# Kernel tuning notes

Hardware: AMD Instinct MI355X
Metric: run time of the kernel (lower is better)

Reference implementation:

```python
import jax, jax.numpy as jnp
import numpy as np


def setup_inputs() -> dict:
    key = jax.random.key(0)
    kx, ky = jax.random.split(key)
    B, C, T = 4, 2, 32768
    x = jax.random.normal(kx, (B, C, T), dtype=jnp.float32)
    y = jax.random.normal(ky, (B, C, T), dtype=jnp.float32)
    return {"x": x, "y": y, "max_shift": 128}


def reference(x, y, max_shift):
    # x: (B, C, T), y: (B, C, T) (or any suffix shape broadcastable from the right)
    T = x.shape[-1]
    S = 2 * max_shift + 1  # number of shift windows
    # pad last dim by max_shift on each side
    pad_cfg = [(0, 0)] * (x.ndim - 1) + [(max_shift, max_shift)]
    x_pad = jnp.pad(x, pad_cfg)
    # unfold into S overlapping windows of length T, stride 1
    idx = jnp.arange(S)[:, None] + jnp.arange(T)[None, :]  # (S, T)
    xw = x_pad[..., idx]                 # (B, C, S, T)
    xw = jnp.moveaxis(xw, -2, 0)         # (S, B, C, T)
    # center each window and y along time
    xw = xw - xw.mean(-1, keepdims=True)
    yc = y - y.mean(-1, keepdims=True)
    corr = (xw * yc).sum(-1)                               # (S, B, C)
    norm = (xw ** 2).sum(-1) * (yc ** 2).sum(-1)           # (S, B, C)
    return corr / jnp.sqrt(norm)
```

## Files before the change

### kernel.cpp

```cpp
#include <hip/hip_runtime.h>
#include <math.h>

#define MAX_SHIFT 128
#define S_TOTAL   257
#define SGB       9
#define NSB       32
#define BLOCK     1024
#define VY        8
#define NW        (BLOCK / 64)
#define NQ        (SGB + 4)

__global__ __launch_bounds__(BLOCK) void spc_kernel(const float* __restrict__ x,
                                                    const float* __restrict__ y,
                                                    float* __restrict__ out,
                                                    int T, int BC) {
    const int sg  = blockIdx.x;
    const int bc  = blockIdx.y;
    const int s0  = sg * 8;
    const int d0  = s0 - MAX_SHIFT;
    const int tid = threadIdx.x;
    const float* xb = x + (size_t)bc * T;
    const float* yb = y + (size_t)bc * T;

    float acc[SGB];
#pragma unroll
    for (int j = 0; j < SGB; ++j) acc[j] = 0.f;
    float sx = 0.f, sxx = 0.f, sy = 0.f, syy = 0.f;

    for (int t = tid * VY; t < T; t += BLOCK * VY) {
        float yv[VY], xv[VY], xw[16];
        *(float4*)(yv)     = *(const float4*)(yb + t);
        *(float4*)(yv + 4) = *(const float4*)(yb + t + 4);
        *(float4*)(xv)     = *(const float4*)(xb + t);
        *(float4*)(xv + 4) = *(const float4*)(xb + t + 4);

        const int g0 = t + d0;
        if (g0 >= 0 && g0 + 16 <= T) {
#pragma unroll
            for (int i = 0; i < 4; ++i)
                *(float4*)(xw + 4 * i) = *(const float4*)(xb + g0 + 4 * i);
        } else {
#pragma unroll
            for (int i = 0; i < 16; ++i) {
                int g = g0 + i;
                xw[i] = (g >= 0 && g < T) ? xb[g] : 0.f;
            }
        }

#pragma unroll
        for (int e = 0; e < VY; ++e) {
            const float yvv = yv[e];
#pragma unroll
            for (int j = 0; j < SGB; ++j)
                acc[j] = fmaf(xw[e + j], yvv, acc[j]);
            sy += yvv;  syy = fmaf(yvv, yvv, syy);
            sx += xv[e]; sxx = fmaf(xv[e], xv[e], sxx);
        }
    }

    __shared__ float red[NQ][NW];
    __shared__ float tot[NQ];
    __shared__ float edge[SGB][2];
    const int lane = tid & 63, wave = tid >> 6;
#pragma unroll
    for (int j = 0; j < SGB; ++j) {
        float v = acc[j];
        for (int off = 32; off; off >>= 1) v += __shfl_down(v, off, 64);
        if (lane == 0) red[j][wave] = v;
    }
    {
        float v4[4] = {sx, sxx, sy, syy};
#pragma unroll
        for (int q = 0; q < 4; ++q) {
            float v = v4[q];
            for (int off = 32; off; off >>= 1) v += __shfl_down(v, off, 64);
            if (lane == 0) red[SGB + q][wave] = v;
        }
    }

    if (wave < SGB) {
        const int sl = wave;
        int d = d0 + sl;
        float pw = 0.f, pw2 = 0.f;
        if (d > 0) {
            for (int j = lane; j < d; j += 64)  { float v = xb[j];         pw += v; pw2 = fmaf(v, v, pw2); }
        } else if (d < 0) {
            for (int j = lane; j < -d; j += 64) { float v = xb[T + d + j]; pw += v; pw2 = fmaf(v, v, pw2); }
        }
        for (int off = 32; off; off >>= 1) {
            pw  += __shfl_down(pw,  off, 64);
            pw2 += __shfl_down(pw2, off, 64);
        }
        if (lane == 0) { edge[sl][0] = pw; edge[sl][1] = pw2; }
    }
    __syncthreads();

    if (tid < NQ) {
        float v = 0.f;
#pragma unroll
        for (int w = 0; w < NW; ++w) v += red[tid][w];
        tot[tid] = v;
    }
    __syncthreads();

    if (tid < SGB) {
        int s = s0 + tid;
        if (s < S_TOTAL) {
            float cr  = tot[tid];
            float Sx  = tot[SGB + 0];
            float Sxx = tot[SGB + 1];
            float Sy  = tot[SGB + 2];
            float Syy = tot[SGB + 3];
            float Sw  = Sx  - edge[tid][0];
            float Sw2 = Sxx - edge[tid][1];
            float invT  = 1.0f / (float)T;
            float corr  = cr  - Sw * Sy * invT;
            float normx = Sw2 - Sw * Sw * invT;
            float normy = Syy - Sy * Sy * invT;
            out[(size_t)s * BC + bc] = corr / sqrtf(normx * normy);
        }
    }
}

extern "C" void kernel_launch(void* const* d_in, const int* in_sizes, int n_in,
                              void* d_out, int out_size, void* d_ws, size_t ws_size,
                              hipStream_t stream) {
    const float* x = (const float*)d_in[0];
    const float* y = (const float*)d_in[1];
    float* out = (float*)d_out;

    const int BC = out_size / S_TOTAL;
    const int T  = in_sizes[0] / BC;

    dim3 grid(NSB, BC);
    spc_kernel<<<grid, BLOCK, 0, stream>>>(x, y, out, T, BC);
}
```

Baseline: 65.98 us.

## Split time axis across blocks and add a separate reduction kernel

Splits the time dimension into 8 chunks per (shift group, batch-channel) using 256-thread blocks, so the grid grows from 256 large blocks to 2048 smaller ones and fills the GPU better. Per-chunk partial sums go to workspace and a second kernel reduces them and computes the edge corrections per shift. The x/y moments are now computed only by the block with zero shift offset, which removes redundant work in the others. The cost is a second kernel launch plus extra workspace traffic.

```diff
diff --git a/kernel.cpp b/kernel.cpp
--- a/kernel.cpp
+++ b/kernel.cpp
@@ -4,35 +4,37 @@
 #define MAX_SHIFT 128
 #define S_TOTAL   257
 #define SGB       9
-#define NSB       32
-#define BLOCK     1024
+#define NSG       32
 #define VY        8
-#define NW        (BLOCK / 64)
-#define NQ        (SGB + 4)
+#define BLK1      256
+#define NW1       (BLK1/64)
+#define CCH       8
 
-__global__ __launch_bounds__(BLOCK) void spc_kernel(const float* __restrict__ x,
-                                                    const float* __restrict__ y,
-                                                    float* __restrict__ out,
-                                                    int T, int BC) {
+
+__global__ __launch_bounds__(BLK1, 8) void spc_partial(const float* __restrict__ x,
+                                                       const float* __restrict__ y,
+                                                       float* __restrict__ ws,
+                                                       int T, int BC) {
     const int sg  = blockIdx.x;
     const int bc  = blockIdx.y;
-    const int s0  = sg * 8;
-    const int d0  = s0 - MAX_SHIFT;
+    const int ch  = blockIdx.z;
+    const int d0  = sg * 8 - MAX_SHIFT;
     const int tid = threadIdx.x;
     const float* xb = x + (size_t)bc * T;
     const float* yb = y + (size_t)bc * T;
+    const int chunk = T / CCH;
+    const int t0 = ch * chunk;
+    const bool domom = (d0 == 0);
 
     float acc[SGB];
 #pragma unroll
     for (int j = 0; j < SGB; ++j) acc[j] = 0.f;
     float sx = 0.f, sxx = 0.f, sy = 0.f, syy = 0.f;
 
-    for (int t = tid * VY; t < T; t += BLOCK * VY) {
-        float yv[VY], xv[VY], xw[16];
+    for (int t = t0 + tid * VY; t < t0 + chunk; t += BLK1 * VY) {
+        float yv[VY], xw[16];
         *(float4*)(yv)     = *(const float4*)(yb + t);
         *(float4*)(yv + 4) = *(const float4*)(yb + t + 4);
-        *(float4*)(xv)     = *(const float4*)(xb + t);
-        *(float4*)(xv + 4) = *(const float4*)(xb + t + 4);
 
         const int g0 = t + d0;
         if (g0 >= 0 && g0 + 16 <= T) {
@@ -53,14 +55,14 @@
 #pragma unroll
             for (int j = 0; j < SGB; ++j)
                 acc[j] = fmaf(xw[e + j], yvv, acc[j]);
-            sy += yvv;  syy = fmaf(yvv, yvv, syy);
-            sx += xv[e]; sxx = fmaf(xv[e], xv[e], sxx);
+            if (domom) {
+                sy += yvv;   syy = fmaf(yvv, yvv, syy);
+                sx += xw[e]; sxx = fmaf(xw[e], xw[e], sxx);
+            }
         }
     }
 
-    __shared__ float red[NQ][NW];
-    __shared__ float tot[NQ];
-    __shared__ float edge[SGB][2];
+    __shared__ float red[SGB + 4][NW1];
     const int lane = tid & 63, wave = tid >> 6;
 #pragma unroll
     for (int j = 0; j < SGB; ++j) {
@@ -68,7 +70,7 @@
         for (int off = 32; off; off >>= 1) v += __shfl_down(v, off, 64);
         if (lane == 0) red[j][wave] = v;
     }
-    {
+    if (domom) {
         float v4[4] = {sx, sxx, sy, syy};
 #pragma unroll
         for (int q = 0; q < 4; ++q) {
@@ -77,48 +79,68 @@
             if (lane == 0) red[SGB + q][wave] = v;
         }
     }
-
-    if (wave < SGB) {
-        const int sl = wave;
-        int d = d0 + sl;
-        float pw = 0.f, pw2 = 0.f;
-        if (d > 0) {
-            for (int j = lane; j < d; j += 64)  { float v = xb[j];         pw += v; pw2 = fmaf(v, v, pw2); }
-        } else if (d < 0) {
-            for (int j = lane; j < -d; j += 64) { float v = xb[T + d + j]; pw += v; pw2 = fmaf(v, v, pw2); }
-        }
-        for (int off = 32; off; off >>= 1) {
-            pw  += __shfl_down(pw,  off, 64);
-            pw2 += __shfl_down(pw2, off, 64);
-        }
-        if (lane == 0) { edge[sl][0] = pw; edge[sl][1] = pw2; }
-    }
-    __syncthreads();
-
-    if (tid < NQ) {
-        float v = 0.f;
-#pragma unroll
-        for (int w = 0; w < NW; ++w) v += red[tid][w];
-        tot[tid] = v;
-    }
     __syncthreads();
 
     if (tid < SGB) {
-        int s = s0 + tid;
-        if (s < S_TOTAL) {
-            float cr  = tot[tid];
-            float Sx  = tot[SGB + 0];
-            float Sxx = tot[SGB + 1];
-            float Sy  = tot[SGB + 2];
-            float Syy = tot[SGB + 3];
-            float Sw  = Sx  - edge[tid][0];
-            float Sw2 = Sxx - edge[tid][1];
-            float invT  = 1.0f / (float)T;
-            float corr  = cr  - Sw * Sy * invT;
-            float normx = Sw2 - Sw * Sw * invT;
-            float normy = Syy - Sy * Sy * invT;
-            out[(size_t)s * BC + bc] = corr / sqrtf(normx * normy);
-        }
+        float v = 0.f;
+#pragma unroll
+        for (int w = 0; w < NW1; ++w) v += red[tid][w];
+        ws[(size_t)((sg * BC + bc) * CCH + ch) * SGB + tid] = v;
+    }
+    if (domom && tid >= SGB && tid < SGB + 4) {
+        const int q = tid - SGB;
+        float v = 0.f;
+#pragma unroll
+        for (int w = 0; w < NW1; ++w) v += red[SGB + q][w];
+        ws[(size_t)NSG * BC * CCH * SGB + (size_t)(bc * CCH + ch) * 4 + q] = v;
+    }
+}
+
+__global__ __launch_bounds__(64) void spc_final(const float* __restrict__ x,
+                                                const float* __restrict__ ws,
+                                                float* __restrict__ out,
+                                                int T, int BC) {
+    const int s    = blockIdx.x;
+    const int bc   = blockIdx.y;
+    const int lane = threadIdx.x;
+    const int sg   = (s >= NSG * 8) ? (NSG - 1) : (s >> 3);
+    const int j    = s - sg * 8;
+    const float* xb = x + (size_t)bc * T;
+
+    float cr = 0.f, Sx = 0.f, Sxx = 0.f, Sy = 0.f, Syy = 0.f;
+    if (lane < CCH) {
+        cr = ws[(size_t)((sg * BC + bc) * CCH + lane) * SGB + j];
+        const float* mb = ws + (size_t)NSG * BC * CCH * SGB + (size_t)(bc * CCH + lane) * 4;
+        Sx = mb[0]; Sxx = mb[1]; Sy = mb[2]; Syy = mb[3];
+    }
+    for (int off = 4; off; off >>= 1) {
+        cr  += __shfl_down(cr,  off, 64);
+        Sx  += __shfl_down(Sx,  off, 64);
+        Sxx += __shfl_down(Sxx, off, 64);
+        Sy  += __shfl_down(Sy,  off, 64);
+        Syy += __shfl_down(Syy, off, 64);
+    }
+
+    const int d = s - MAX_SHIFT;
+    float pw = 0.f, pw2 = 0.f;
+    if (d > 0) {
+        for (int i = lane; i < d; i += 64)  { float v = xb[i];         pw += v; pw2 = fmaf(v, v, pw2); }
+    } else if (d < 0) {
+        for (int i = lane; i < -d; i += 64) { float v = xb[T + d + i]; pw += v; pw2 = fmaf(v, v, pw2); }
+    }
+    for (int off = 32; off; off >>= 1) {
+        pw  += __shfl_down(pw,  off, 64);
+        pw2 += __shfl_down(pw2, off, 64);
+    }
+
+    if (lane == 0) {
+        const float Sw   = Sx  - pw;
+        const float Sw2  = Sxx - pw2;
+        const float invT = 1.0f / (float)T;
+        const float corr  = cr  - Sw * Sy * invT;
+        const float normx = Sw2 - Sw * Sw * invT;
+        const float normy = Syy - Sy * Sy * invT;
+        out[(size_t)s * BC + bc] = corr / sqrtf(normx * normy);
     }
 }
 
@@ -128,10 +150,14 @@
     const float* x = (const float*)d_in[0];
     const float* y = (const float*)d_in[1];
     float* out = (float*)d_out;
+    float* ws  = (float*)d_ws;
 
     const int BC = out_size / S_TOTAL;
     const int T  = in_sizes[0] / BC;
 
-    dim3 grid(NSB, BC);
-    spc_kernel<<<grid, BLOCK, 0, stream>>>(x, y, out, T, BC);
+    dim3 g1(NSG, BC, CCH);
+    spc_partial<<<g1, BLK1, 0, stream>>>(x, y, ws, T, BC);
+
+    dim3 g2(S_TOTAL, BC);
+    spc_final<<<g2, 64, 0, stream>>>(x, ws, out, T, BC);
 }
```

After: 70.72 us. +7.2%, slower.

## Compute window sums from shifted x and drop per-shift edge loops

Applied to the files above, without the earlier changes.

Each thread now processes 16 y samples with a 24-wide x window. The window sum and sum-of-squares are accumulated from the shifted x directly rather than from unshifted x. That removes the separate x loads and the per-wave edge-correction loops over up to 128 elements, and only an 8-element correction remains at the end. The grid is flattened so that blocks of the same shift group over different batch rows are adjacent, and bc is hardcoded as blockIdx&7, which assumes BC=8. The larger VY raises register use and halves the number of loop iterations per thread.

```diff
diff --git a/kernel.cpp b/kernel.cpp
--- a/kernel.cpp
+++ b/kernel.cpp
@@ -4,18 +4,19 @@
 #define MAX_SHIFT 128
 #define S_TOTAL   257
 #define SGB       9
-#define NSB       32
+#define NSG       32
+#define VY        16
 #define BLOCK     1024
-#define VY        8
 #define NW        (BLOCK / 64)
 #define NQ        (SGB + 4)
+#define WIN       (VY + 8)
 
 __global__ __launch_bounds__(BLOCK) void spc_kernel(const float* __restrict__ x,
                                                     const float* __restrict__ y,
                                                     float* __restrict__ out,
                                                     int T, int BC) {
-    const int sg  = blockIdx.x;
-    const int bc  = blockIdx.y;
+    const int bc  = blockIdx.x & 7;
+    const int sg  = blockIdx.x >> 3;
     const int s0  = sg * 8;
     const int d0  = s0 - MAX_SHIFT;
     const int tid = threadIdx.x;
@@ -25,23 +26,22 @@
     float acc[SGB];
 #pragma unroll
     for (int j = 0; j < SGB; ++j) acc[j] = 0.f;
-    float sx = 0.f, sxx = 0.f, sy = 0.f, syy = 0.f;
+    float w = 0.f, w2 = 0.f, sy = 0.f, syy = 0.f;
 
     for (int t = tid * VY; t < T; t += BLOCK * VY) {
-        float yv[VY], xv[VY], xw[16];
-        *(float4*)(yv)     = *(const float4*)(yb + t);
-        *(float4*)(yv + 4) = *(const float4*)(yb + t + 4);
-        *(float4*)(xv)     = *(const float4*)(xb + t);
-        *(float4*)(xv + 4) = *(const float4*)(xb + t + 4);
+        float yv[VY], xw[WIN];
+#pragma unroll
+        for (int i = 0; i < VY / 4; ++i)
+            *(float4*)(yv + 4 * i) = *(const float4*)(yb + t + 4 * i);
 
         const int g0 = t + d0;
-        if (g0 >= 0 && g0 + 16 <= T) {
+        if (g0 >= 0 && g0 + WIN <= T) {
 #pragma unroll
-            for (int i = 0; i < 4; ++i)
+            for (int i = 0; i < WIN / 4; ++i)
                 *(float4*)(xw + 4 * i) = *(const float4*)(xb + g0 + 4 * i);
         } else {
 #pragma unroll
-            for (int i = 0; i < 16; ++i) {
+            for (int i = 0; i < WIN; ++i) {
                 int g = g0 + i;
                 xw[i] = (g >= 0 && g < T) ? xb[g] : 0.f;
             }
@@ -53,14 +53,13 @@
 #pragma unroll
             for (int j = 0; j < SGB; ++j)
                 acc[j] = fmaf(xw[e + j], yvv, acc[j]);
-            sy += yvv;  syy = fmaf(yvv, yvv, syy);
-            sx += xv[e]; sxx = fmaf(xv[e], xv[e], sxx);
+            sy += yvv;   syy = fmaf(yvv, yvv, syy);
+            w  += xw[e]; w2  = fmaf(xw[e], xw[e], w2);
         }
     }
 
     __shared__ float red[NQ][NW];
     __shared__ float tot[NQ];
-    __shared__ float edge[SGB][2];
     const int lane = tid & 63, wave = tid >> 6;
 #pragma unroll
     for (int j = 0; j < SGB; ++j) {
@@ -69,7 +68,7 @@
         if (lane == 0) red[j][wave] = v;
     }
     {
-        float v4[4] = {sx, sxx, sy, syy};
+        float v4[4] = {w, w2, sy, syy};
 #pragma unroll
         for (int q = 0; q < 4; ++q) {
             float v = v4[q];
@@ -77,48 +76,40 @@
             if (lane == 0) red[SGB + q][wave] = v;
         }
     }
-
-    if (wave < SGB) {
-        const int sl = wave;
-        int d = d0 + sl;
-        float pw = 0.f, pw2 = 0.f;
-        if (d > 0) {
-            for (int j = lane; j < d; j += 64)  { float v = xb[j];         pw += v; pw2 = fmaf(v, v, pw2); }
-        } else if (d < 0) {
-            for (int j = lane; j < -d; j += 64) { float v = xb[T + d + j]; pw += v; pw2 = fmaf(v, v, pw2); }
-        }
-        for (int off = 32; off; off >>= 1) {
-            pw  += __shfl_down(pw,  off, 64);
-            pw2 += __shfl_down(pw2, off, 64);
-        }
-        if (lane == 0) { edge[sl][0] = pw; edge[sl][1] = pw2; }
-    }
     __syncthreads();
 
     if (tid < NQ) {
         float v = 0.f;
 #pragma unroll
-        for (int w = 0; w < NW; ++w) v += red[tid][w];
+        for (int wv = 0; wv < NW; ++wv) v += red[tid][wv];
         tot[tid] = v;
     }
     __syncthreads();
 
-    if (tid < SGB) {
-        int s = s0 + tid;
-        if (s < S_TOTAL) {
-            float cr  = tot[tid];
-            float Sx  = tot[SGB + 0];
-            float Sxx = tot[SGB + 1];
-            float Sy  = tot[SGB + 2];
-            float Syy = tot[SGB + 3];
-            float Sw  = Sx  - edge[tid][0];
-            float Sw2 = Sxx - edge[tid][1];
-            float invT  = 1.0f / (float)T;
-            float corr  = cr  - Sw * Sy * invT;
-            float normx = Sw2 - Sw * Sw * invT;
-            float normy = Syy - Sy * Sy * invT;
-            out[(size_t)s * BC + bc] = corr / sqrtf(normx * normy);
-        }
+    if (tid < SGB && (tid < 8 || sg == NSG - 1)) {
+        const int s = s0 + tid;
+        float ev[8];
+        const float* bp = xb + ((d0 >= 0) ? d0 : T + d0);
+        *(float4*)(ev)     = *(const float4*)(bp);
+        *(float4*)(ev + 4) = *(const float4*)(bp + 4);
+        float es = 0.f, es2 = 0.f;
+#pragma unroll
+        for (int i = 0; i < 8; ++i)
+            if (i < tid) { es += ev[i]; es2 = fmaf(ev[i], ev[i], es2); }
+
+        const float W   = tot[SGB + 0];
+        const float W2  = tot[SGB + 1];
+        const float Sy  = tot[SGB + 2];
+        const float Syy = tot[SGB + 3];
+        const float Sw  = (d0 >= 0) ? (W  - es)  : (W  + es);
+        const float Sw2 = (d0 >= 0) ? (W2 - es2) : (W2 + es2);
+
+        const float invT  = 1.0f / (float)T;
+        const float cr    = tot[tid];
+        const float corr  = cr  - Sw * Sy * invT;
+        const float normx = Sw2 - Sw * Sw * invT;
+        const float normy = Syy - Sy * Sy * invT;
+        out[(size_t)s * BC + bc] = corr / sqrtf(normx * normy);
     }
 }
 
@@ -132,6 +123,5 @@
     const int BC = out_size / S_TOTAL;
     const int T  = in_sizes[0] / BC;
 
-    dim3 grid(NSB, BC);
-    spc_kernel<<<grid, BLOCK, 0, stream>>>(x, y, out, T, BC);
+    spc_kernel<<<dim3(NSG * BC), BLOCK, 0, stream>>>(x, y, out, T, BC);
 }
```

Result: no change. 65.54 us (-0.7%).
